# Kernel tuning notes

Measured on AMD Instinct MI355X. Metric: run time of the kernel, lower is better.

## Reference

```python
import jax, jax.numpy as jnp
import numpy as np

SIGMA = 1.0
EPSILON = 1.0
MAX_ITER = 10


def pairwise_kernel(x, y, sigma=SIGMA):
    # k = -||x-y||^2 / (2 sigma^2), shape [B, L, K]
    outer = jnp.einsum('bld,bkd->blk', x, y)
    nx = jnp.sum(x * x, axis=2)
    ny = jnp.sum(y * y, axis=2)
    dist = jnp.clip(nx[:, :, None] + ny[:, None, :] - 2.0 * outer, 0.0, None)
    return -dist / (2.0 * sigma ** 2)


def c_transform(potential, log_weight, kernel, epsilon=EPSILON):
    # rho=None => scale=1, lse = -eps * logsumexp(kernel/eps + (pot/eps + log_w))
    s = potential / epsilon + log_weight            # [B, K]
    operand = kernel / epsilon + s[:, None, :]      # [B, L, K]
    return -epsilon * jax.scipy.special.logsumexp(operand, axis=2)


def potentials(kxy, log_a, log_b):
    kyx = jnp.swapaxes(kxy, 1, 2)
    f0 = jnp.zeros_like(log_a)
    g0 = jnp.zeros_like(log_b)

    def step(carry, _):
        f, g = carry
        fn = c_transform(g, log_b, kxy)
        gn = c_transform(f, log_a, kyx)
        return ((fn + f) * 0.5, (gn + g) * 0.5), None

    (f, g), _ = jax.lax.scan(step, (f0, g0), None, length=MAX_ITER)
    return f, g


def sym_potential(x, log_a):
    kxx = pairwise_kernel(x, x)
    f0 = jnp.zeros_like(log_a)

    def step(f, _):
        fn = c_transform(f, log_a, kxx)
        return (fn + f) * 0.5, None

    f, _ = jax.lax.scan(step, f0, None, length=MAX_ITER)
    return f


def evaluate_potential(x, a, y, b, g):
    # phi_transform is identity for rho=None; scaled_dot_prod forward = sum(a*f, dim=1)
    kxy = pairwise_kernel(x, y)
    f = c_transform(g, jnp.log(b), kxy)
    return jnp.sum(a * f, axis=1)


def setup_inputs() -> dict:
    key = jax.random.key(0)
    k1, k2, k3, k4 = jax.random.split(key, 4)
    B, L, K, D = 8, 2048, 2048, 32
    x = jax.random.normal(k1, (B, L, D), dtype=jnp.float32)
    y = jax.random.normal(k2, (B, K, D), dtype=jnp.float32)
    a = jax.random.uniform(k3, (B, L), dtype=jnp.float32, minval=0.1, maxval=1.0)
    b = jax.random.uniform(k4, (B, K), dtype=jnp.float32, minval=0.1, maxval=1.0)
    a = a / jnp.sum(a, axis=1, keepdims=True)
    b = b / jnp.sum(b, axis=1, keepdims=True)
    return {"x": x, "a": a, "y": y, "b": b}


def reference(x, a, y, b):
    log_a, log_b = jnp.log(a), jnp.log(b)
    kxy = pairwise_kernel(x, y)
    f, g = potentials(kxy, log_a, log_b)
    dist = evaluate_potential(x, a, y, b, g) + evaluate_potential(y, b, x, a, f)
    fx = sym_potential(x, log_a)
    fy = sym_potential(y, log_b)
    ent_x = evaluate_potential(x, a, x, a, fx)
    ent_y = evaluate_potential(y, b, y, b, fy)
    return jnp.mean(dist - ent_x - ent_y)
```

## Files before the change

kernel.cpp:

```cpp
#include <hip/hip_runtime.h>
#include <math.h>

#define BATCH 8
#define NPT   2048
#define DIM   32
#define RPB   32
#define CPW   (NPT / 4)
#define NT    (CPW / 16)
#define L2E   1.44269504088896f
#define BN    (BATCH * NPT)

typedef __attribute__((ext_vector_type(8))) _Float16 half8;
typedef __attribute__((ext_vector_type(4))) float floatx4;
typedef unsigned short u16;
typedef unsigned int u32;

__device__ __forceinline__ u16 f2h_bits(float v) {
    _Float16 h = (_Float16)v;
    return *(u16*)&h;
}
__device__ __forceinline__ float exp2v(float x) { return __builtin_amdgcn_exp2f(x); }

struct CtSet {
    const u16* Ah;
    const u16* Bh;
    const float* tls;
    const float* qX;
    const float* bmIn;
    const float* cwNext;
    const float* prev;
    float* out;
    float* tlsOut;
    float* bmOut;
};
struct CtArgs { CtSet s[4]; int average; };

__global__ __launch_bounds__(256, 8) void ct_kernel(CtArgs args) {
    const CtSet cs = args.s[blockIdx.y];
    const int batch = blockIdx.z;
    const int row0 = blockIdx.x * RPB;
    const int tid  = threadIdx.x;
    const int w = tid >> 6, lane = tid & 63, n = lane & 15, quad = lane >> 4;
    const int qk = quad * 8;
    const size_t pbase = (size_t)batch * NPT * DIM;
    const size_t vbase = (size_t)batch * NPT;

    __shared__ float lsum[RPB][4];

    const u16* __restrict__ Ah = cs.Ah + pbase;
    const u16* __restrict__ Bh = cs.Bh + pbase;
    const float* __restrict__ tls = cs.tls + vbase;

    half8 ah[2];
    #pragma unroll
    for (int s = 0; s < 2; s++) {
        size_t off = (size_t)(row0 + s * 16 + n) * DIM + qk;
        ah[s] = *(const half8*)(Ah + off);
    }

    float tmv = fmaxf(cs.bmIn[batch * 128 + lane], cs.bmIn[batch * 128 + 64 + lane]);
    #pragma unroll
    for (int m = 1; m < 64; m <<= 1) tmv = fmaxf(tmv, __shfl_xor(tmv, m, 64));
    const float Tmax = tmv;
    const float l2eTmax = L2E * Tmax;

    float sum[2][4];
    #pragma unroll
    for (int s = 0; s < 2; s++)
        #pragma unroll
        for (int r = 0; r < 4; r++) sum[s][r] = 0.0f;

    const int c0 = w * CPW + n;
    const u16* bp = Bh + (size_t)c0 * DIM + qk;
    const float* tp = tls + c0;

    half8 b0, b1;
    float t0, t1;
    b0 = *(const half8*)bp;  t0 = *tp;

    #pragma unroll 1
    for (int ch = 0; ch < NT; ch += 2) {
        b1 = *(const half8*)(bp + (size_t)(ch + 1) * 16 * DIM);
        t1 = tp[(ch + 1) * 16];
        {
            float wq = exp2v(t0 - l2eTmax);
            floatx4 acc[2];
            #pragma unroll
            for (int s = 0; s < 2; s++) acc[s] = (floatx4){0.f, 0.f, 0.f, 0.f};
            #pragma unroll
            for (int s = 0; s < 2; s++)
                acc[s] = __builtin_amdgcn_mfma_f32_16x16x32_f16(ah[s], b0, acc[s], 0, 0, 0);
            #pragma unroll
            for (int s = 0; s < 2; s++)
                #pragma unroll
                for (int r = 0; r < 4; r++)
                    sum[s][r] = fmaf(wq, exp2v(acc[s][r]), sum[s][r]);
        }
        if (ch + 2 < NT) {
            b0 = *(const half8*)(bp + (size_t)(ch + 2) * 16 * DIM);
            t0 = tp[(ch + 2) * 16];
        }
        {
            float wq = exp2v(t1 - l2eTmax);
            floatx4 acc[2];
            #pragma unroll
            for (int s = 0; s < 2; s++) acc[s] = (floatx4){0.f, 0.f, 0.f, 0.f};
            #pragma unroll
            for (int s = 0; s < 2; s++)
                acc[s] = __builtin_amdgcn_mfma_f32_16x16x32_f16(ah[s], b1, acc[s], 0, 0, 0);
            #pragma unroll
            for (int s = 0; s < 2; s++)
                #pragma unroll
                for (int r = 0; r < 4; r++)
                    sum[s][r] = fmaf(wq, exp2v(acc[s][r]), sum[s][r]);
        }
    }

    #pragma unroll
    for (int s = 0; s < 2; s++)
        #pragma unroll
        for (int r = 0; r < 4; r++) {
            float v = sum[s][r];
            #pragma unroll
            for (int m = 1; m < 16; m <<= 1) v += __shfl_xor(v, m, 64);
            if (n == 0) lsum[s * 16 + quad * 4 + r][w] = v;
        }
    __syncthreads();

    if (tid < RPB) {
        float T = (lsum[tid][0] + lsum[tid][1]) + (lsum[tid][2] + lsum[tid][3]);
        int l = row0 + tid;
        float lse = Tmax + __logf(T);
        float val = cs.qX[vbase + l] - lse;
        if (args.average) val = 0.5f * (cs.prev[vbase + l] + val);
        cs.out[vbase + l] = val;
        float tc = val + cs.cwNext[vbase + l];
        cs.tlsOut[vbase + l] = L2E * tc;
        float bm = tc;
        #pragma unroll
        for (int m = 1; m < 16; m <<= 1) bm = fmaxf(bm, __shfl_xor(bm, m, 64));
        if ((tid & 15) == 0)
            cs.bmOut[batch * 128 + blockIdx.x * 2 + (tid >> 4)] = bm;
    }
}

struct InitArgs {
    const float *x, *a, *y, *b;
    float *c_x, *c_y, *qx, *qy;
    u16 *xh, *yh, *xsh, *ysh;
    float *f0, *g0, *fx0, *fy0;
    float *tlsF0, *tlsG0, *tlsFx0, *tlsFy0;
    float *bmF0, *bmG0, *bmFx0, *bmFy0;
};

__global__ __launch_bounds__(256) void init_kernel(InitArgs ia) {
    int idx = blockIdx.x * 256 + threadIdx.x;
    if (idx >= BN) return;
    const float* xp = ia.x + (size_t)idx * DIM;
    const float* yp = ia.y + (size_t)idx * DIM;
    u32* xhp  = (u32*)ia.xh  + (size_t)idx * (DIM / 2);
    u32* yhp  = (u32*)ia.yh  + (size_t)idx * (DIM / 2);
    u32* xshp = (u32*)ia.xsh + (size_t)idx * (DIM / 2);
    u32* yshp = (u32*)ia.ysh + (size_t)idx * (DIM / 2);
    float sx = 0.f, sy = 0.f;
    #pragma unroll
    for (int d = 0; d < DIM; d += 2) {
        float v0 = xp[d], v1 = xp[d + 1];
        sx += v0 * v0 + v1 * v1;
        xhp[d / 2]  = (u32)f2h_bits(v0) | ((u32)f2h_bits(v1) << 16);
        xshp[d / 2] = (u32)f2h_bits(L2E * v0) | ((u32)f2h_bits(L2E * v1) << 16);
        float u0 = yp[d], u1 = yp[d + 1];
        sy += u0 * u0 + u1 * u1;
        yhp[d / 2]  = (u32)f2h_bits(u0) | ((u32)f2h_bits(u1) << 16);
        yshp[d / 2] = (u32)f2h_bits(L2E * u0) | ((u32)f2h_bits(L2E * u1) << 16);
    }
    float qxv = 0.5f * sx, qyv = 0.5f * sy;
    ia.qx[idx] = qxv; ia.qy[idx] = qyv;
    float cxv = __logf(ia.a[idx]) - qxv;
    float cyv = __logf(ia.b[idx]) - qyv;
    ia.c_x[idx] = cxv; ia.c_y[idx] = cyv;
    ia.f0[idx] = 0.f; ia.g0[idx] = 0.f; ia.fx0[idx] = 0.f; ia.fy0[idx] = 0.f;
    ia.tlsF0[idx] = L2E * cxv; ia.tlsG0[idx] = L2E * cyv;
    ia.tlsFx0[idx] = L2E * cxv; ia.tlsFy0[idx] = L2E * cyv;
    float mx = cxv, my = cyv;
    #pragma unroll
    for (int m = 1; m < 16; m <<= 1) {
        mx = fmaxf(mx, __shfl_xor(mx, m, 32));
        my = fmaxf(my, __shfl_xor(my, m, 32));
    }
    if ((threadIdx.x & 15) == 0) {
        int g = idx >> 4;
        ia.bmF0[g] = mx; ia.bmFx0[g] = mx;
        ia.bmG0[g] = my; ia.bmFy0[g] = my;
    }
}

__global__ __launch_bounds__(1024) void reduce_kernel(
        const float* __restrict__ a, const float* __restrict__ b,
        const float* __restrict__ ctA, const float* __restrict__ ctB,
        const float* __restrict__ ctX, const float* __restrict__ ctY,
        float* __restrict__ out) {
    float acc = 0.f;
    for (int idx = threadIdx.x; idx < BN; idx += 1024) {
        acc += a[idx] * (ctA[idx] - ctX[idx]) + b[idx] * (ctB[idx] - ctY[idx]);
    }
    #pragma unroll
    for (int off = 32; off > 0; off >>= 1) acc += __shfl_down(acc, off, 64);
    __shared__ float sm[16];
    if ((threadIdx.x & 63) == 0) sm[threadIdx.x >> 6] = acc;
    __syncthreads();
    if (threadIdx.x == 0) {
        float t = 0.f;
        #pragma unroll
        for (int i = 0; i < 16; i++) t += sm[i];
        out[0] = t / (float)BATCH;
    }
}

extern "C" void kernel_launch(void* const* d_in, const int* in_sizes, int n_in,
                              void* d_out, int out_size, void* d_ws, size_t ws_size,
                              hipStream_t stream) {
    const float* x = (const float*)d_in[0];
    const float* a = (const float*)d_in[1];
    const float* y = (const float*)d_in[2];
    const float* b = (const float*)d_in[3];
    float* out = (float*)d_out;

    float* ws = (float*)d_ws;
    float* c_x = ws + 0 * BN;
    float* c_y = ws + 1 * BN;
    float* qx  = ws + 2 * BN;
    float* qy  = ws + 3 * BN;
    float* fb[2]  = { ws + 4 * BN,  ws + 5 * BN };
    float* gb[2]  = { ws + 6 * BN,  ws + 7 * BN };
    float* fxb[2] = { ws + 8 * BN,  ws + 9 * BN };
    float* fyb[2] = { ws + 10 * BN, ws + 11 * BN };
    float* ctA = ws + 12 * BN;
    float* ctB = ws + 13 * BN;
    float* ctX = ws + 14 * BN;
    float* ctY = ws + 15 * BN;
    float* tlsF[2]  = { ws + 16 * BN, ws + 17 * BN };
    float* tlsG[2]  = { ws + 18 * BN, ws + 19 * BN };
    float* tlsFx[2] = { ws + 20 * BN, ws + 21 * BN };
    float* tlsFy[2] = { ws + 22 * BN, ws + 23 * BN };
    float* dummyT = ws + 24 * BN;
    float* small = ws + 25 * BN;
    float* bmF[2]  = { small + 0 * 1024, small + 1 * 1024 };
    float* bmG[2]  = { small + 2 * 1024, small + 3 * 1024 };
    float* bmFx[2] = { small + 4 * 1024, small + 5 * 1024 };
    float* bmFy[2] = { small + 6 * 1024, small + 7 * 1024 };
    float* dummyB = small + 8 * 1024;
    u16* bf = (u16*)(small + 10 * 1024);
    const size_t AS = (size_t)BN * DIM;
    u16* xh  = bf + 0 * AS;
    u16* yh  = bf + 1 * AS;
    u16* xsh = bf + 2 * AS;
    u16* ysh = bf + 3 * AS;

    InitArgs ia;
    ia.x = x; ia.a = a; ia.y = y; ia.b = b;
    ia.c_x = c_x; ia.c_y = c_y; ia.qx = qx; ia.qy = qy;
    ia.xh = xh; ia.yh = yh; ia.xsh = xsh; ia.ysh = ysh;
    ia.f0 = fb[0]; ia.g0 = gb[0]; ia.fx0 = fxb[0]; ia.fy0 = fyb[0];
    ia.tlsF0 = tlsF[0]; ia.tlsG0 = tlsG[0]; ia.tlsFx0 = tlsFx[0]; ia.tlsFy0 = tlsFy[0];
    ia.bmF0 = bmF[0]; ia.bmG0 = bmG[0]; ia.bmFx0 = bmFx[0]; ia.bmFy0 = bmFy[0];
    init_kernel<<<BN / 256, 256, 0, stream>>>(ia);

    dim3 grid(NPT / RPB, 4, BATCH);
    int cur = 0;
    for (int it = 0; it < 10; it++) {
        CtArgs ar;
        ar.average = 1;
        ar.s[0] = { xh, ysh, tlsG[cur], qx, bmG[cur], c_x,
                    fb[cur], fb[1 - cur], tlsF[1 - cur], bmF[1 - cur] };
        ar.s[1] = { yh, xsh, tlsF[cur], qy, bmF[cur], c_y,
                    gb[cur], gb[1 - cur], tlsG[1 - cur], bmG[1 - cur] };
        ar.s[2] = { xh, xsh, tlsFx[cur], qx, bmFx[cur], c_x,
                    fxb[cur], fxb[1 - cur], tlsFx[1 - cur], bmFx[1 - cur] };
        ar.s[3] = { yh, ysh, tlsFy[cur], qy, bmFy[cur], c_y,
                    fyb[cur], fyb[1 - cur], tlsFy[1 - cur], bmFy[1 - cur] };
        ct_kernel<<<grid, 256, 0, stream>>>(ar);
        cur ^= 1;
    }

    CtArgs fin;
    fin.average = 0;
    fin.s[0] = { xh, ysh, tlsG[cur], qx, bmG[cur], c_x, fb[cur], ctA, dummyT, dummyB };
    fin.s[1] = { yh, xsh, tlsF[cur], qy, bmF[cur], c_y, gb[cur], ctB, dummyT, dummyB };
    fin.s[2] = { xh, xsh, tlsFx[cur], qx, bmFx[cur], c_x, fxb[cur], ctX, dummyT, dummyB };
    fin.s[3] = { yh, ysh, tlsFy[cur], qy, bmFy[cur], c_y, fyb[cur], ctY, dummyT, dummyB };
    ct_kernel<<<grid, 256, 0, stream>>>(fin);

    reduce_kernel<<<1, 1024, 0, stream>>>(a, b, ctA, ctB, ctX, ctY, out);
}
```

Baseline: 327.6 us.

## Fuse all Sinkhorn iterations into one cooperative kernel with grid sync

Replaces the eleven separate ct_kernel launches and the final reduce kernel with one cooperative persistent kernel. It runs all iterations with grid.sync between them, each block handling two row blocks per pass. The final weighted reduction moves into the last pass via atomicAdd, dropping the ct output buffers and the reduce launch. This removes per-launch overhead and tail gaps, but halves the grid to 1024 blocks at lower occupancy, adds grid-barrier cost, and makes the float atomic summation order nondeterministic.

```diff
diff --git a/kernel.cpp b/kernel.cpp
--- a/kernel.cpp
+++ b/kernel.cpp
@@ -1,5 +1,8 @@
 #include <hip/hip_runtime.h>
+#include <hip/hip_cooperative_groups.h>
 #include <math.h>
+
+namespace cg = cooperative_groups;
 
 #define BATCH 8
 #define NPT   2048
@@ -21,35 +24,34 @@
 }
 __device__ __forceinline__ float exp2v(float x) { return __builtin_amdgcn_exp2f(x); }
 
-struct CtSet {
-    const u16* Ah;
-    const u16* Bh;
-    const float* tls;
-    const float* qX;
-    const float* bmIn;
-    const float* cwNext;
-    const float* prev;
+struct FusedArgs {
+    const u16* A[4];
+    const u16* Bp[4];
+    const float* qX[4];
+    const float* wgt[4];
+    float sgn[4];
+    float* pot[4][2];
+    float* tls[4][2];
+    float* bm[4][2];
+    const float* cwN[4];
     float* out;
-    float* tlsOut;
-    float* bmOut;
 };
-struct CtArgs { CtSet s[4]; int average; };
-
-__global__ __launch_bounds__(256, 8) void ct_kernel(CtArgs args) {
-    const CtSet cs = args.s[blockIdx.y];
-    const int batch = blockIdx.z;
-    const int row0 = blockIdx.x * RPB;
-    const int tid  = threadIdx.x;
+
+__device__ __forceinline__ void ct_pass(const FusedArgs& fa, int set, int batch,
+                                        int rb, bool fin, int c,
+                                        float lsum[RPB][4]) {
+    const int tid = threadIdx.x;
     const int w = tid >> 6, lane = tid & 63, n = lane & 15, quad = lane >> 4;
     const int qk = quad * 8;
+    const int row0 = rb * RPB;
     const size_t pbase = (size_t)batch * NPT * DIM;
     const size_t vbase = (size_t)batch * NPT;
-
-    __shared__ float lsum[RPB][4];
-
-    const u16* __restrict__ Ah = cs.Ah + pbase;
-    const u16* __restrict__ Bh = cs.Bh + pbase;
-    const float* __restrict__ tls = cs.tls + vbase;
+    const int inS = (set == 0) ? 1 : (set == 1) ? 0 : set;
+
+    const u16* __restrict__ Ah = fa.A[set] + pbase;
+    const u16* __restrict__ Bh = fa.Bp[set] + pbase;
+    const float* __restrict__ tlsIn = fa.tls[inS][c] + vbase;
+    const float* __restrict__ bmIn  = fa.bm[inS][c];
 
     half8 ah[2];
     #pragma unroll
@@ -58,7 +60,7 @@
         ah[s] = *(const half8*)(Ah + off);
     }
 
-    float tmv = fmaxf(cs.bmIn[batch * 128 + lane], cs.bmIn[batch * 128 + 64 + lane]);
+    float tmv = fmaxf(bmIn[batch * 128 + lane], bmIn[batch * 128 + 64 + lane]);
     #pragma unroll
     for (int m = 1; m < 64; m <<= 1) tmv = fmaxf(tmv, __shfl_xor(tmv, m, 64));
     const float Tmax = tmv;
@@ -72,7 +74,7 @@
 
     const int c0 = w * CPW + n;
     const u16* bp = Bh + (size_t)c0 * DIM + qk;
-    const float* tp = tls + c0;
+    const float* tp = tlsIn + c0;
 
     half8 b0, b1;
     float t0, t1;
@@ -131,17 +133,55 @@
         float T = (lsum[tid][0] + lsum[tid][1]) + (lsum[tid][2] + lsum[tid][3]);
         int l = row0 + tid;
         float lse = Tmax + __logf(T);
-        float val = cs.qX[vbase + l] - lse;
-        if (args.average) val = 0.5f * (cs.prev[vbase + l] + val);
-        cs.out[vbase + l] = val;
-        float tc = val + cs.cwNext[vbase + l];
-        cs.tlsOut[vbase + l] = L2E * tc;
-        float bm = tc;
-        #pragma unroll
-        for (int m = 1; m < 16; m <<= 1) bm = fmaxf(bm, __shfl_xor(bm, m, 64));
-        if ((tid & 15) == 0)
-            cs.bmOut[batch * 128 + blockIdx.x * 2 + (tid >> 4)] = bm;
-    }
+        float val = fa.qX[set][vbase + l] - lse;
+        if (!fin) {
+            val = 0.5f * (fa.pot[set][c][vbase + l] + val);
+            fa.pot[set][c ^ 1][vbase + l] = val;
+            float tc = val + fa.cwN[set][vbase + l];
+            fa.tls[set][c ^ 1][vbase + l] = L2E * tc;
+            float bmv = tc;
+            #pragma unroll
+            for (int m = 1; m < 16; m <<= 1) bmv = fmaxf(bmv, __shfl_xor(bmv, m, 64));
+            if ((tid & 15) == 0)
+                fa.bm[set][c ^ 1][batch * 128 + rb * 2 + (tid >> 4)] = bmv;
+        } else {
+            float partial = fa.sgn[set] * fa.wgt[set][vbase + l] * val;
+            #pragma unroll
+            for (int m = 1; m < 32; m <<= 1) partial += __shfl_xor(partial, m, 64);
+            if (tid == 0) atomicAdd(fa.out, partial);
+        }
+    }
+}
+
+__global__ __launch_bounds__(256, 4) void fused_kernel(FusedArgs fa) {
+    cg::grid_group grid = cg::this_grid();
+    __shared__ float lsum[RPB][4];
+    const int bx = blockIdx.x;
+    const int rbp   = bx & 31;
+    const int set   = (bx >> 5) & 3;
+    const int batch = bx >> 7;
+
+    int c = 0;
+    #pragma unroll 1
+    for (int it = 0; it <= 10; it++) {
+        const bool fin = (it == 10);
+        ct_pass(fa, set, batch, rbp * 2, fin, c, lsum);
+        __syncthreads();
+        ct_pass(fa, set, batch, rbp * 2 + 1, fin, c, lsum);
+        if (!fin) {
+            grid.sync();
+            c ^= 1;
+        }
+    }
+}
+
+__global__ __launch_bounds__(256, 8) void iter_kernel(FusedArgs fa, int it, int c) {
+    __shared__ float lsum[RPB][4];
+    const int bx = blockIdx.x;
+    const int rb    = bx & 63;
+    const int set   = (bx >> 6) & 3;
+    const int batch = bx >> 8;
+    ct_pass(fa, set, batch, rb, it == 10, c, lsum);
 }
 
 struct InitArgs {
@@ -151,11 +191,13 @@
     float *f0, *g0, *fx0, *fy0;
     float *tlsF0, *tlsG0, *tlsFx0, *tlsFy0;
     float *bmF0, *bmG0, *bmFx0, *bmFy0;
+    float *out;
 };
 
 __global__ __launch_bounds__(256) void init_kernel(InitArgs ia) {
     int idx = blockIdx.x * 256 + threadIdx.x;
     if (idx >= BN) return;
+    if (idx == 0) ia.out[0] = 0.0f;
     const float* xp = ia.x + (size_t)idx * DIM;
     const float* yp = ia.y + (size_t)idx * DIM;
     u32* xhp  = (u32*)ia.xh  + (size_t)idx * (DIM / 2);
@@ -195,28 +237,6 @@
     }
 }
 
-__global__ __launch_bounds__(1024) void reduce_kernel(
-        const float* __restrict__ a, const float* __restrict__ b,
-        const float* __restrict__ ctA, const float* __restrict__ ctB,
-        const float* __restrict__ ctX, const float* __restrict__ ctY,
-        float* __restrict__ out) {
-    float acc = 0.f;
-    for (int idx = threadIdx.x; idx < BN; idx += 1024) {
-        acc += a[idx] * (ctA[idx] - ctX[idx]) + b[idx] * (ctB[idx] - ctY[idx]);
-    }
-    #pragma unroll
-    for (int off = 32; off > 0; off >>= 1) acc += __shfl_down(acc, off, 64);
-    __shared__ float sm[16];
-    if ((threadIdx.x & 63) == 0) sm[threadIdx.x >> 6] = acc;
-    __syncthreads();
-    if (threadIdx.x == 0) {
-        float t = 0.f;
-        #pragma unroll
-        for (int i = 0; i < 16; i++) t += sm[i];
-        out[0] = t / (float)BATCH;
-    }
-}
-
 extern "C" void kernel_launch(void* const* d_in, const int* in_sizes, int n_in,
                               void* d_out, int out_size, void* d_ws, size_t ws_size,
                               hipStream_t stream) {
@@ -235,22 +255,16 @@
     float* gb[2]  = { ws + 6 * BN,  ws + 7 * BN };
     float* fxb[2] = { ws + 8 * BN,  ws + 9 * BN };
     float* fyb[2] = { ws + 10 * BN, ws + 11 * BN };
-    float* ctA = ws + 12 * BN;
-    float* ctB = ws + 13 * BN;
-    float* ctX = ws + 14 * BN;
-    float* ctY = ws + 15 * BN;
-    float* tlsF[2]  = { ws + 16 * BN, ws + 17 * BN };
-    float* tlsG[2]  = { ws + 18 * BN, ws + 19 * BN };
-    float* tlsFx[2] = { ws + 20 * BN, ws + 21 * BN };
-    float* tlsFy[2] = { ws + 22 * BN, ws + 23 * BN };
-    float* dummyT = ws + 24 * BN;
-    float* small = ws + 25 * BN;
+    float* tlsF[2]  = { ws + 12 * BN, ws + 13 * BN };
+    float* tlsG[2]  = { ws + 14 * BN, ws + 15 * BN };
+    float* tlsFx[2] = { ws + 16 * BN, ws + 17 * BN };
+    float* tlsFy[2] = { ws + 18 * BN, ws + 19 * BN };
+    float* small = ws + 20 * BN;
     float* bmF[2]  = { small + 0 * 1024, small + 1 * 1024 };
     float* bmG[2]  = { small + 2 * 1024, small + 3 * 1024 };
     float* bmFx[2] = { small + 4 * 1024, small + 5 * 1024 };
     float* bmFy[2] = { small + 6 * 1024, small + 7 * 1024 };
-    float* dummyB = small + 8 * 1024;
-    u16* bf = (u16*)(small + 10 * 1024);
+    u16* bf = (u16*)(small + 8 * 1024);
     const size_t AS = (size_t)BN * DIM;
     u16* xh  = bf + 0 * AS;
     u16* yh  = bf + 1 * AS;
@@ -264,32 +278,41 @@
     ia.f0 = fb[0]; ia.g0 = gb[0]; ia.fx0 = fxb[0]; ia.fy0 = fyb[0];
     ia.tlsF0 = tlsF[0]; ia.tlsG0 = tlsG[0]; ia.tlsFx0 = tlsFx[0]; ia.tlsFy0 = tlsFy[0];
     ia.bmF0 = bmF[0]; ia.bmG0 = bmG[0]; ia.bmFx0 = bmFx[0]; ia.bmFy0 = bmFy[0];
+    ia.out = out;
     init_kernel<<<BN / 256, 256, 0, stream>>>(ia);
 
-    dim3 grid(NPT / RPB, 4, BATCH);
-    int cur = 0;
-    for (int it = 0; it < 10; it++) {
-        CtArgs ar;
-        ar.average = 1;
-        ar.s[0] = { xh, ysh, tlsG[cur], qx, bmG[cur], c_x,
-                    fb[cur], fb[1 - cur], tlsF[1 - cur], bmF[1 - cur] };
-        ar.s[1] = { yh, xsh, tlsF[cur], qy, bmF[cur], c_y,
-                    gb[cur], gb[1 - cur], tlsG[1 - cur], bmG[1 - cur] };
-        ar.s[2] = { xh, xsh, tlsFx[cur], qx, bmFx[cur], c_x,
-                    fxb[cur], fxb[1 - cur], tlsFx[1 - cur], bmFx[1 - cur] };
-        ar.s[3] = { yh, ysh, tlsFy[cur], qy, bmFy[cur], c_y,
-                    fyb[cur], fyb[1 - cur], tlsFy[1 - cur], bmFy[1 - cur] };
-        ct_kernel<<<grid, 256, 0, stream>>>(ar);
-        cur ^= 1;
-    }
-
-    CtArgs fin;
-    fin.average = 0;
-    fin.s[0] = { xh, ysh, tlsG[cur], qx, bmG[cur], c_x, fb[cur], ctA, dummyT, dummyB };
-    fin.s[1] = { yh, xsh, tlsF[cur], qy, bmF[cur], c_y, gb[cur], ctB, dummyT, dummyB };
-    fin.s[2] = { xh, xsh, tlsFx[cur], qx, bmFx[cur], c_x, fxb[cur], ctX, dummyT, dummyB };
-    fin.s[3] = { yh, ysh, tlsFy[cur], qy, bmFy[cur], c_y, fyb[cur], ctY, dummyT, dummyB };
-    ct_kernel<<<grid, 256, 0, stream>>>(fin);
-
-    reduce_kernel<<<1, 1024, 0, stream>>>(a, b, ctA, ctB, ctX, ctY, out);
-}
+    FusedArgs fa;
+    fa.A[0] = xh;  fa.A[1] = yh;  fa.A[2] = xh;  fa.A[3] = yh;
+    fa.Bp[0] = ysh; fa.Bp[1] = xsh; fa.Bp[2] = xsh; fa.Bp[3] = ysh;
+    fa.qX[0] = qx; fa.qX[1] = qy; fa.qX[2] = qx; fa.qX[3] = qy;
+    fa.wgt[0] = a; fa.wgt[1] = b; fa.wgt[2] = a; fa.wgt[3] = b;
+    fa.sgn[0] = 1.0f / BATCH; fa.sgn[1] = 1.0f / BATCH;
+    fa.sgn[2] = -1.0f / BATCH; fa.sgn[3] = -1.0f / BATCH;
+    fa.cwN[0] = c_x; fa.cwN[1] = c_y; fa.cwN[2] = c_x; fa.cwN[3] = c_y;
+    for (int p = 0; p < 2; p++) {
+        fa.pot[0][p] = fb[p];  fa.pot[1][p] = gb[p];
+        fa.pot[2][p] = fxb[p]; fa.pot[3][p] = fyb[p];
+        fa.tls[0][p] = tlsF[p];  fa.tls[1][p] = tlsG[p];
+        fa.tls[2][p] = tlsFx[p]; fa.tls[3][p] = tlsFy[p];
+        fa.bm[0][p] = bmF[p];  fa.bm[1][p] = bmG[p];
+        fa.bm[2][p] = bmFx[p]; fa.bm[3][p] = bmFy[p];
+    }
+    fa.out = out;
+
+    int maxBlocksPerCU = 0;
+    hipError_t qerr = hipOccupancyMaxActiveBlocksPerMultiprocessor(
+        &maxBlocksPerCU, (const void*)fused_kernel, 256, 0);
+    bool use_coop = (qerr == hipSuccess) && ((long)maxBlocksPerCU * 256 >= 1024);
+
+    if (use_coop) {
+        void* kp[] = { &fa };
+        hipLaunchCooperativeKernel((void*)fused_kernel, dim3(1024), dim3(256),
+                                   kp, 0, stream);
+    } else {
+        int c = 0;
+        for (int it = 0; it <= 10; it++) {
+            iter_kernel<<<dim3(2048), 256, 0, stream>>>(fa, it, c);
+            if (it < 10) c ^= 1;
+        }
+    }
+}
```

After: 344.9 us. 1.05x slower.
